# Kernel optimization log

Hardware: AMD Instinct MI355X
Metric: run time of the kernel (lower is better)

## Reference

```python
import jax, jax.numpy as jnp
import numpy as np
from jax import lax

T, B, A = 128, 32, 18  # rollout steps, num envs, action dim
HID = 128
FEAT = 512


def _conv(x, w, b, stride):
    y = lax.conv_general_dilated(x, w, (stride, stride), 'VALID',
                                 dimension_numbers=('NCHW', 'OIHW', 'NCHW'))
    return y + b[None, :, None, None]


def setup_inputs() -> dict:
    key = jax.random.key(0)
    ks = jax.random.split(key, 16)

    def w(k, shape, fan_in):
        return jax.random.normal(k, shape, dtype=jnp.float32) / np.sqrt(fan_in)

    x = jax.random.uniform(ks[0], (T * B, 4, 84, 84), dtype=jnp.float32) * 255.0
    done = jax.random.randint(ks[1], (T * B,), 0, 2, dtype=jnp.int32)
    h0 = jax.random.normal(ks[2], (1, B, HID), dtype=jnp.float32) * 0.1
    c0 = jax.random.normal(ks[3], (1, B, HID), dtype=jnp.float32) * 0.1
    return {
        'x': x, 'done': done, 'h0': h0, 'c0': c0,
        'w1': w(ks[4], (32, 4, 8, 8), 4 * 64), 'b1': jnp.zeros((32,), jnp.float32),
        'w2': w(ks[5], (64, 32, 4, 4), 32 * 16), 'b2': jnp.zeros((64,), jnp.float32),
        'w3': w(ks[6], (64, 64, 3, 3), 64 * 9), 'b3': jnp.zeros((64,), jnp.float32),
        'wf': w(ks[7], (FEAT, 3136), 3136), 'bf': jnp.zeros((FEAT,), jnp.float32),
        'w_ih': w(ks[8], (4 * HID, FEAT), FEAT), 'w_hh': w(ks[9], (4 * HID, HID), HID),
        'b_ih': jnp.zeros((4 * HID,), jnp.float32), 'b_hh': jnp.zeros((4 * HID,), jnp.float32),
        'wa': w(ks[10], (A, HID), HID) * 0.01, 'ba': jnp.zeros((A,), jnp.float32),
        'wc': w(ks[11], (1, HID), HID), 'bc': jnp.zeros((1,), jnp.float32),
    }


def reference(x, done, h0, c0, w1, b1, w2, b2, w3, b3, wf, bf,
              w_ih, w_hh, b_ih, b_hh, wa, ba, wc, bc):
    # Nature-CNN trunk on x/255
    h = jax.nn.relu(_conv(x / 255.0, w1, b1, 4))   # (TB,32,20,20)
    h = jax.nn.relu(_conv(h, w2, b2, 2))           # (TB,64,9,9)
    h = jax.nn.relu(_conv(h, w3, b3, 1))           # (TB,64,7,7)
    h = h.reshape(h.shape[0], -1)                   # (TB,3136)
    feat = jax.nn.relu(h @ wf.T + bf)               # (TB,512)

    xs = feat.reshape(T, B, FEAT)
    ds = done.reshape(T, B).astype(feat.dtype)

    def step(carry, inp):
        hh, cc = carry
        xt, dt = inp
        m = (1.0 - dt)[:, None]      # done-mask reset of recurrent state
        hh = hh * m
        cc = cc * m
        gates = xt @ w_ih.T + b_ih + hh @ w_hh.T + b_hh
        i, f, g, o = jnp.split(gates, 4, axis=-1)  # torch LSTM gate order
        cc = jax.nn.sigmoid(f) * cc + jax.nn.sigmoid(i) * jnp.tanh(g)
        hh = jax.nn.sigmoid(o) * jnp.tanh(cc)
        return (hh, cc), hh

    (_, _), hs = lax.scan(step, (h0[0], c0[0]), (xs, ds))
    hidden = hs.reshape(T * B, HID)

    logits = hidden @ wa.T + ba                     # actor head
    value = hidden @ wc.T + bc                      # critic head
    return jnp.concatenate([logits, value], axis=-1)  # (TB, A+1)
```

## Files before the change

### kernel.cpp

```cpp
#include <hip/hip_runtime.h>

typedef _Float16 f16;
typedef _Float16 f16x2 __attribute__((ext_vector_type(2)));
typedef _Float16 f16x4 __attribute__((ext_vector_type(4)));
typedef _Float16 f16x8 __attribute__((ext_vector_type(8)));
typedef float f32x4 __attribute__((ext_vector_type(4)));

__device__ __forceinline__ float sigf(float x){ return 1.f/(1.f + __expf(-x)); }
__device__ __forceinline__ float tanhfast(float x){ return 2.f/(1.f + __expf(-2.f*x)) - 1.f; }
__device__ __forceinline__ float fdot2f(f16x2 a, f16x2 b, float c){
#if __has_builtin(__builtin_amdgcn_fdot2)
  return __builtin_amdgcn_fdot2(a, b, c, false);
#else
  return c + (float)a.x*(float)b.x + (float)a.y*(float)b.y;
#endif
}

__global__ void prep_w1(const float* __restrict__ w, f16* __restrict__ dst){
  int idx = blockIdx.x*256 + threadIdx.x;
  if (idx >= 8192) return;
  int och = idx >> 8, rem = idx & 255;
  int c = rem >> 6, ky = (rem >> 3) & 7, kx = rem & 7;
  int k = c*64 + ky*8 + kx;
  dst[(k>>3)*256 + och*8 + (k&7)] = (f16)(w[idx] * (1.f/255.f));
}
__global__ void prep_w2(const float* __restrict__ w, f16* __restrict__ dst){
  int idx = blockIdx.x*256 + threadIdx.x;
  if (idx >= 32768) return;
  int och = idx >> 9;
  int c = (idx >> 4) & 31, ky = (idx >> 2) & 3, kx = idx & 3;
  int k = (ky*4 + kx)*32 + c;
  dst[(k>>3)*512 + och*8 + (k&7)] = (f16)w[idx];
}
__global__ void prep_w3(const float* __restrict__ w, f16* __restrict__ dst){
  int idx = blockIdx.x*256 + threadIdx.x;
  if (idx >= 36864) return;
  int och = idx / 576, r = idx % 576;
  int c = r / 9, r2 = r % 9;
  int ky = r2 / 3, kx = r2 % 3;
  int k = (ky*3 + kx)*64 + c;
  dst[(k>>3)*512 + och*8 + (k&7)] = (f16)w[idx];
}
__global__ void prep_wf(const float* __restrict__ w, f16* __restrict__ dst){
  int idx = blockIdx.x*256 + threadIdx.x;
  if (idx >= 392*512*8) return;
  int j = idx & 7, n = (idx >> 3) & 511, k8 = idx >> 12;
  int kf = k8*8 + j;
  int c = kf & 63, p = kf >> 6;
  dst[idx] = (f16)w[(size_t)n*3136 + c*49 + p];
}
__global__ void prep_wih(const float* __restrict__ w, f16* __restrict__ dst){
  int idx = blockIdx.x*256 + threadIdx.x;
  if (idx >= 262144) return;
  int j = idx & 7, n = (idx >> 3) & 511, k8 = idx >> 12;
  dst[idx] = (f16)w[n*512 + k8*8 + j];
}
__global__ void prep_wheads(const float* __restrict__ wa, const float* __restrict__ wc,
                            f16* __restrict__ dst){
  int idx = blockIdx.x*256 + threadIdx.x;
  if (idx >= 4096) return;
  int n = idx >> 7, k = idx & 127;
  float v = 0.f;
  if (n < 18) v = wa[n*128 + k];
  else if (n == 18) v = wc[k];
  dst[(k>>3)*256 + n*8 + (k&7)] = (f16)v;
}
__global__ void prep_bsum(const float* __restrict__ a, const float* __restrict__ b,
                          float* __restrict__ s){
  int i = blockIdx.x*256 + threadIdx.x;
  if (i < 512) s[i] = a[i] + b[i];
}
__global__ void prep_whh(const float* __restrict__ w, f16* __restrict__ dst){
  int idx = blockIdx.x*256 + threadIdx.x;
  if (idx >= 65536) return;
  int nn = idx >> 7, k = idx & 127;
  dst[(k >> 1)*1024 + nn*2 + (k & 1)] = (f16)w[idx];
}

__global__ __launch_bounds__(256, 3) void conv123_k(const float* __restrict__ x,
    const f16* __restrict__ Bp1, const float* __restrict__ b1,
    const f16* __restrict__ Bp2, const float* __restrict__ b2,
    const f16* __restrict__ Bp3, const float* __restrict__ b3,
    f16* __restrict__ y3){
  __shared__ alignas(16) f16 xt[4*24*84];
  __shared__ alignas(16) f16 y1t[400*32];
  int n = blockIdx.x;
  int tid = threadIdx.x;
  int lane = tid & 63, w = tid >> 6;
  int q = lane >> 4, m = lane & 15;

  int wg = w & 1, wm = w >> 1;
  int och1 = wg*16 + m;
  f16x8 bfr1[8];
  #pragma unroll
  for (int s = 0; s < 8; ++s)
    bfr1[s] = *(const f16x8*)(Bp1 + ((4*s + q)*32 + och1)*8);
  float bias1 = b1[och1];

  #pragma unroll
  for (int h = 0; h < 4; ++h){
    for (int i = tid; i < 2016; i += 256){
      int c = i / 504, r = i % 504;
      int iy = r / 21, x4 = r % 21;
      const float4* xp = (const float4*)(x + (((size_t)n*4 + c)*84 + h*20 + iy)*84) + x4;
      float4 v = *xp;
      f16x4 hv = { (f16)v.x, (f16)v.y, (f16)v.z, (f16)v.w };
      *(f16x4*)(&xt[(c*24 + iy)*84 + x4*4]) = hv;
    }
    __syncthreads();
    int oy4[4], ox4[4];
    #pragma unroll
    for (int i = 0; i < 4; ++i){
      int pl = i*16 + m; if (pl > 49) pl = 49;
      int p = wm*50 + pl;
      oy4[i] = (p/20)*4; ox4[i] = (p%20)*4;
    }
    f32x4 acc1[4] = {};
    #pragma unroll
    for (int s = 0; s < 8; ++s){
      int k8 = 4*s + q;
      int c = k8 >> 3, ky = k8 & 7;
      #pragma unroll
      for (int i = 0; i < 4; ++i){
        const f16* ap = &xt[(c*24 + oy4[i] + ky)*84 + ox4[i]];
        f16x4 lo = *(const f16x4*)ap;
        f16x4 hi = *(const f16x4*)(ap + 4);
        f16x8 a = __builtin_shufflevector(lo, hi, 0,1,2,3,4,5,6,7);
        acc1[i] = __builtin_amdgcn_mfma_f32_16x16x32_f16(a, bfr1[s], acc1[i], 0, 0, 0);
      }
    }
    #pragma unroll
    for (int i = 0; i < 4; ++i)
      #pragma unroll
      for (int r = 0; r < 4; ++r){
        int pl = i*16 + q*4 + r;
        if (pl < 50){
          int P = h*100 + wm*50 + pl;
          float v = acc1[i][r] + bias1; v = v > 0.f ? v : 0.f;
          int idx = (P*32 + och1) ^ (((P>>1)&7)<<3);
          y1t[idx] = (f16)v;
        }
      }
    __syncthreads();
  }

  int och2 = w*16 + m;
  f16x8 bfr2[16];
  #pragma unroll
  for (int s = 0; s < 16; ++s)
    bfr2[s] = *(const f16x8*)(Bp2 + ((size_t)(4*s + q)*64 + och2)*8);
  int basev[6];
  #pragma unroll
  for (int i = 0; i < 6; ++i){
    int px = i*16 + m; if (px > 80) px = 80;
    basev[i] = (px/9*2)*20 + (px%9)*2;
  }
  f32x4 acc2[6] = {};
  #pragma unroll
  for (int s = 0; s < 16; ++s){
    int k8 = 4*s + q;
    int c0 = (k8 & 3)*8;
    int kk = k8 >> 2;
    int poff = (kk >> 2)*20 + (kk & 3);
    #pragma unroll
    for (int i = 0; i < 6; ++i){
      int p = basev[i] + poff;
      int idx = (p*32 + c0) ^ (((p>>1)&7)<<3);
      f16x8 a = *(const f16x8*)(&y1t[idx]);
      acc2[i] = __builtin_amdgcn_mfma_f32_16x16x32_f16(a, bfr2[s], acc2[i], 0, 0, 0);
    }
  }
  float bias2 = b2[och2];
  #pragma unroll
  for (int i = 0; i < 6; ++i)
    #pragma unroll
    for (int r = 0; r < 4; ++r){
      int px = i*16 + q*4 + r;
      if (px < 81){
        float v = acc2[i][r] + bias2; v = v > 0.f ? v : 0.f;
        int idx = (px*64 + och2) ^ ((px&7)<<3);
        xt[idx] = (f16)v;
      }
    }
  __syncthreads();

  int basev3[4];
  #pragma unroll
  for (int i = 0; i < 4; ++i){
    int px = i*16 + m; if (px > 48) px = 48;
    basev3[i] = (px/7)*9 + (px%7);
  }
  f32x4 acc3[4] = {};
  for (int s = 0; s < 18; ++s){
    int k8 = 4*s + q;
    int c0 = (k8 & 7)*8;
    int kxy = k8 >> 3;
    int ky = kxy/3, kx = kxy%3;
    f16x8 b = *(const f16x8*)(Bp3 + ((size_t)k8*64 + och2)*8);
    int poff = ky*9 + kx;
    #pragma unroll
    for (int i = 0; i < 4; ++i){
      int p = basev3[i] + poff;
      int idx = (p*64 + c0) ^ ((p&7)<<3);
      f16x8 a = *(const f16x8*)(&xt[idx]);
      acc3[i] = __builtin_amdgcn_mfma_f32_16x16x32_f16(a, b, acc3[i], 0, 0, 0);
    }
  }
  float bias3 = b3[och2];
  #pragma unroll
  for (int i = 0; i < 4; ++i)
    #pragma unroll
    for (int r = 0; r < 4; ++r){
      int px = i*16 + q*4 + r;
      if (px < 49){
        float v = acc3[i][r] + bias3; v = v > 0.f ? v : 0.f;
        y3[((size_t)n*49 + px)*64 + och2] = (f16)v;
      }
    }
}

template<bool RELU, bool OUTH>
__global__ __launch_bounds__(256) void gemm_k(const f16* __restrict__ A,
    const f16* __restrict__ Bp, const float* __restrict__ bias, void* __restrict__ out,
    int M, int N, int K){
  __shared__ alignas(16) f16 at[64*264];
  int m0 = blockIdx.x*64, n0 = blockIdx.y*64;
  int lane = threadIdx.x & 63, w = threadIdx.x >> 6;
  int q = lane >> 4, cl = lane & 15;
  int mh = w >> 1, nh = w & 1;
  f32x4 acc[2][2] = {};
  for (int kb = 0; kb < K; kb += 256){
    int kblen = K - kb; if (kblen > 256) kblen = 256;
    int c8n = kblen >> 3;
    __syncthreads();
    int tot = 64*c8n;
    for (int i = threadIdx.x; i < tot; i += 256){
      int row, c8;
      if (c8n == 32){ row = i >> 5; c8 = i & 31; } else { row = i >> 3; c8 = i & 7; }
      *(f16x8*)(&at[row*264 + c8*8]) = *(const f16x8*)(&A[(size_t)(m0+row)*K + kb + c8*8]);
    }
    __syncthreads();
    int nks = kblen >> 5;
    for (int s = 0; s < nks; ++s){
      f16x8 a[2], b[2];
      #pragma unroll
      for (int mi = 0; mi < 2; ++mi)
        a[mi] = *(const f16x8*)(&at[((mh*2+mi)*16 + cl)*264 + 32*s + 8*q]);
      #pragma unroll
      for (int ni = 0; ni < 2; ++ni){
        int nn = n0 + (nh*2+ni)*16 + cl;
        b[ni] = *(const f16x8*)(&Bp[((size_t)((kb>>3) + 4*s + q)*N + nn)*8]);
      }
      #pragma unroll
      for (int mi = 0; mi < 2; ++mi)
        #pragma unroll
        for (int ni = 0; ni < 2; ++ni)
          acc[mi][ni] = __builtin_amdgcn_mfma_f32_16x16x32_f16(a[mi], b[ni], acc[mi][ni], 0,0,0);
    }
  }
  #pragma unroll
  for (int ni = 0; ni < 2; ++ni){
    int nn = n0 + (nh*2+ni)*16 + cl;
    float bv = bias[nn];
    #pragma unroll
    for (int mi = 0; mi < 2; ++mi)
      #pragma unroll
      for (int r = 0; r < 4; ++r){
        int mg = m0 + (mh*2+mi)*16 + q*4 + r;
        float v = acc[mi][ni][r] + bv;
        if (RELU) v = v > 0.f ? v : 0.f;
        if (OUTH) ((f16*)out)[(size_t)mg*N + nn] = (f16)v;
        else      ((float*)out)[(size_t)mg*N + nn] = v;
      }
  }
}

__global__ __launch_bounds__(128) void lstm_seg(const float* __restrict__ gx,
    const f16* __restrict__ whhT2, const int* __restrict__ done,
    const float* __restrict__ h0, const float* __restrict__ c0,
    f16* __restrict__ hs){
  int e = blockIdx.y, t0 = blockIdx.x;
  if (t0 > 0 && done[t0*32 + e] == 0) return;
  int j = threadIdx.x;
  __shared__ f16 hl[2][128];
  float h, c;
  if (t0 == 0){
    float mm = 1.f - (float)done[e];
    h = h0[e*128 + j]*mm;
    c = c0[e*128 + j]*mm;
  } else { h = 0.f; c = 0.f; }
  int buf = 0;
  hl[0][j] = (f16)h;
  __syncthreads();
  const f16x2* wp = (const f16x2*)whhT2;
  for (int t = t0; t < 128; ++t){
    if (t > t0 && done[t*32 + e] != 0) break;
    const float* gxr = gx + ((size_t)t*32 + e)*512;
    float gi = gxr[j], gf = gxr[128 + j], gg = gxr[256 + j], go = gxr[384 + j];
    const f16x2* hp = (const f16x2*)hl[buf];
    float ai = 0.f, af = 0.f, ag = 0.f, ao = 0.f;
    #pragma unroll 8
    for (int k2 = 0; k2 < 64; ++k2){
      f16x2 hv = hp[k2];
      const f16x2* wr = wp + k2*512;
      ai = fdot2f(wr[j], hv, ai);
      af = fdot2f(wr[128 + j], hv, af);
      ag = fdot2f(wr[256 + j], hv, ag);
      ao = fdot2f(wr[384 + j], hv, ao);
    }
    gi += ai; gf += af; gg += ag; go += ao;
    c = sigf(gf)*c + sigf(gi)*tanhfast(gg);
    h = sigf(go)*tanhfast(c);
    hs[((size_t)t*32 + e)*128 + j] = (f16)h;
    buf ^= 1;
    hl[buf][j] = (f16)h;
    __syncthreads();
  }
}

__global__ __launch_bounds__(256) void heads_k(const f16* __restrict__ hs,
    const f16* __restrict__ Bp, const float* __restrict__ ba, const float* __restrict__ bc,
    float* __restrict__ out){
  __shared__ alignas(16) f16 at[64*128];
  int m0 = blockIdx.x*64;
  for (int i = threadIdx.x; i < 1024; i += 256)
    ((uint4*)at)[i] = ((const uint4*)(hs + (size_t)m0*128))[i];
  int lane = threadIdx.x & 63, w = threadIdx.x >> 6;
  int q = lane >> 4, cl = lane & 15;
  __syncthreads();
  f32x4 acc[2] = {};
  #pragma unroll
  for (int s = 0; s < 4; ++s){
    f16x8 a = *(const f16x8*)(&at[(w*16 + cl)*128 + 32*s + 8*q]);
    #pragma unroll
    for (int nt = 0; nt < 2; ++nt){
      f16x8 b = *(const f16x8*)(&Bp[((4*s + q)*32 + nt*16 + cl)*8]);
      acc[nt] = __builtin_amdgcn_mfma_f32_16x16x32_f16(a, b, acc[nt], 0,0,0);
    }
  }
  #pragma unroll
  for (int nt = 0; nt < 2; ++nt){
    int n = nt*16 + cl;
    if (n < 19){
      float bv = (n < 18) ? ba[n] : bc[0];
      #pragma unroll
      for (int r = 0; r < 4; ++r){
        int m = m0 + w*16 + q*4 + r;
        out[(size_t)m*19 + n] = acc[nt][r] + bv;
      }
    }
  }
}

extern "C" void kernel_launch(void* const* d_in, const int* in_sizes, int n_in,
                              void* d_out, int out_size, void* d_ws, size_t ws_size,
                              hipStream_t stream){
  const float* x   = (const float*)d_in[0];
  const int*   dn  = (const int*)d_in[1];
  const float* h0  = (const float*)d_in[2];
  const float* c0  = (const float*)d_in[3];
  const float* w1  = (const float*)d_in[4];
  const float* b1  = (const float*)d_in[5];
  const float* w2  = (const float*)d_in[6];
  const float* b2  = (const float*)d_in[7];
  const float* w3  = (const float*)d_in[8];
  const float* b3  = (const float*)d_in[9];
  const float* wf  = (const float*)d_in[10];
  const float* bf  = (const float*)d_in[11];
  const float* wih = (const float*)d_in[12];
  const float* whh = (const float*)d_in[13];
  const float* bih = (const float*)d_in[14];
  const float* bhh = (const float*)d_in[15];
  const float* wa  = (const float*)d_in[16];
  const float* ba  = (const float*)d_in[17];
  const float* wc  = (const float*)d_in[18];
  const float* bc  = (const float*)d_in[19];
  float* out = (float*)d_out;

  char* ws = (char*)d_ws;
  size_t off = 0;
  auto alloc = [&](size_t bytes)->char*{
    char* p = ws + off;
    off += (bytes + 255) & ~(size_t)255;
    return p;
  };
  f16*  y3   = (f16*)alloc(4096UL*3136*2);
  f16*  feat = (f16*)alloc(4096UL*512*2);
  float* gx  = (float*)alloc(4096UL*512*4);
  f16*  hs   = (f16*)alloc(4096UL*128*2);
  f16*  Bp1  = (f16*)alloc(32UL*32*8*2);
  f16*  Bp2  = (f16*)alloc(64UL*64*8*2);
  f16*  Bp3  = (f16*)alloc(72UL*64*8*2);
  f16*  Bpf  = (f16*)alloc(392UL*512*8*2);
  f16*  Bpih = (f16*)alloc(64UL*512*8*2);
  f16*  Bph  = (f16*)alloc(16UL*32*8*2);
  float* bsum = (float*)alloc(512UL*4);
  f16*  whhT2 = (f16*)alloc(64UL*512*2*2);

  prep_w1<<<32, 256, 0, stream>>>(w1, Bp1);
  prep_w2<<<128, 256, 0, stream>>>(w2, Bp2);
  prep_w3<<<144, 256, 0, stream>>>(w3, Bp3);
  prep_wf<<<6272, 256, 0, stream>>>(wf, Bpf);
  prep_wih<<<1024, 256, 0, stream>>>(wih, Bpih);
  prep_wheads<<<16, 256, 0, stream>>>(wa, wc, Bph);
  prep_bsum<<<2, 256, 0, stream>>>(bih, bhh, bsum);
  prep_whh<<<256, 256, 0, stream>>>(whh, whhT2);

  conv123_k<<<4096, 256, 0, stream>>>(x, Bp1, b1, Bp2, b2, Bp3, b3, y3);
  gemm_k<true,  true ><<<dim3(64, 8), 256, 0, stream>>>(y3,   Bpf,  bf,   (void*)feat, 4096, 512, 3136);
  gemm_k<false, false><<<dim3(64, 8), 256, 0, stream>>>(feat, Bpih, bsum, (void*)gx,   4096, 512, 512);
  lstm_seg<<<dim3(128, 32), 128, 0, stream>>>(gx, whhT2, dn, h0, c0, hs);
  heads_k<<<64, 256, 0, stream>>>(hs, Bph, ba, bc, out);
}
```

Baseline: 897.6 us.

## Prefetch conv1 input bands into registers and vectorize conv epilogue stores

The fused conv kernel now loads the next 20-row input band into registers while the current band is computed, so global-load latency overlaps MFMA work instead of stalling each band. MFMA operands are swapped so each lane holds four consecutive output channels, which lets the bias+ReLU epilogues write packed f16x4 to LDS and global memory instead of scalar f16 stores. The cost is 8 float4 registers per thread held across the loop, which may pressure occupancy at launch bounds of 3 blocks.

```diff
diff --git a/kernel.cpp b/kernel.cpp
--- a/kernel.cpp
+++ b/kernel.cpp
@@ -88,32 +88,52 @@
   int tid = threadIdx.x;
   int lane = tid & 63, w = tid >> 6;
   int q = lane >> 4, m = lane & 15;
-
   int wg = w & 1, wm = w >> 1;
+  const float* xn = x + (size_t)n*4*84*84;
+
+  float4 fl[8];
+  #pragma unroll
+  for (int u = 0; u < 8; ++u){
+    int i = tid + u*256; if (i > 2015) i = 2015;
+    int c = i / 504, r = i % 504;
+    int iy = r / 21, x4 = r % 21;
+    fl[u] = *((const float4*)(xn + (c*84 + iy)*84) + x4);
+  }
   int och1 = wg*16 + m;
   f16x8 bfr1[8];
   #pragma unroll
   for (int s = 0; s < 8; ++s)
     bfr1[s] = *(const f16x8*)(Bp1 + ((4*s + q)*32 + och1)*8);
-  float bias1 = b1[och1];
+  f32x4 bias1v = *(const f32x4*)(b1 + wg*16 + q*4);
 
   #pragma unroll
   for (int h = 0; h < 4; ++h){
-    for (int i = tid; i < 2016; i += 256){
+    __syncthreads();
+    #pragma unroll
+    for (int u = 0; u < 8; ++u){
+      int i = tid + u*256; if (i > 2015) i = 2015;
       int c = i / 504, r = i % 504;
       int iy = r / 21, x4 = r % 21;
-      const float4* xp = (const float4*)(x + (((size_t)n*4 + c)*84 + h*20 + iy)*84) + x4;
-      float4 v = *xp;
+      float4 v = fl[u];
       f16x4 hv = { (f16)v.x, (f16)v.y, (f16)v.z, (f16)v.w };
       *(f16x4*)(&xt[(c*24 + iy)*84 + x4*4]) = hv;
     }
+    if (h < 3){
+      #pragma unroll
+      for (int u = 0; u < 8; ++u){
+        int i = tid + u*256; if (i > 2015) i = 2015;
+        int c = i / 504, r = i % 504;
+        int iy = r / 21, x4 = r % 21;
+        fl[u] = *((const float4*)(xn + (c*84 + (h+1)*20 + iy)*84) + x4);
+      }
+    }
     __syncthreads();
     int oy4[4], ox4[4];
     #pragma unroll
-    for (int i = 0; i < 4; ++i){
-      int pl = i*16 + m; if (pl > 49) pl = 49;
+    for (int i2 = 0; i2 < 4; ++i2){
+      int pl = i2*16 + m; if (pl > 49) pl = 49;
       int p = wm*50 + pl;
-      oy4[i] = (p/20)*4; ox4[i] = (p%20)*4;
+      oy4[i2] = (p/20)*4; ox4[i2] = (p%20)*4;
     }
     f32x4 acc1[4] = {};
     #pragma unroll
@@ -121,28 +141,31 @@
       int k8 = 4*s + q;
       int c = k8 >> 3, ky = k8 & 7;
       #pragma unroll
-      for (int i = 0; i < 4; ++i){
-        const f16* ap = &xt[(c*24 + oy4[i] + ky)*84 + ox4[i]];
+      for (int i2 = 0; i2 < 4; ++i2){
+        const f16* ap = &xt[(c*24 + oy4[i2] + ky)*84 + ox4[i2]];
         f16x4 lo = *(const f16x4*)ap;
         f16x4 hi = *(const f16x4*)(ap + 4);
         f16x8 a = __builtin_shufflevector(lo, hi, 0,1,2,3,4,5,6,7);
-        acc1[i] = __builtin_amdgcn_mfma_f32_16x16x32_f16(a, bfr1[s], acc1[i], 0, 0, 0);
-      }
-    }
-    #pragma unroll
-    for (int i = 0; i < 4; ++i)
-      #pragma unroll
-      for (int r = 0; r < 4; ++r){
-        int pl = i*16 + q*4 + r;
-        if (pl < 50){
-          int P = h*100 + wm*50 + pl;
-          float v = acc1[i][r] + bias1; v = v > 0.f ? v : 0.f;
-          int idx = (P*32 + och1) ^ (((P>>1)&7)<<3);
-          y1t[idx] = (f16)v;
+        acc1[i2] = __builtin_amdgcn_mfma_f32_16x16x32_f16(bfr1[s], a, acc1[i2], 0, 0, 0);
+      }
+    }
+    #pragma unroll
+    for (int i2 = 0; i2 < 4; ++i2){
+      int pl = i2*16 + m;
+      if (pl < 50){
+        int P = h*100 + wm*50 + pl;
+        f16x4 hv;
+        #pragma unroll
+        for (int r = 0; r < 4; ++r){
+          float v = acc1[i2][r] + bias1v[r]; v = v > 0.f ? v : 0.f;
+          hv[r] = (f16)v;
         }
-      }
-    __syncthreads();
-  }
+        int idx = (P*32 + wg*16 + q*4) ^ (((P>>1)&7)<<3);
+        *(f16x4*)(&y1t[idx]) = hv;
+      }
+    }
+  }
+  __syncthreads();
 
   int och2 = w*16 + m;
   f16x8 bfr2[16];
@@ -167,21 +190,24 @@
       int p = basev[i] + poff;
       int idx = (p*32 + c0) ^ (((p>>1)&7)<<3);
       f16x8 a = *(const f16x8*)(&y1t[idx]);
-      acc2[i] = __builtin_amdgcn_mfma_f32_16x16x32_f16(a, bfr2[s], acc2[i], 0, 0, 0);
-    }
-  }
-  float bias2 = b2[och2];
-  #pragma unroll
-  for (int i = 0; i < 6; ++i)
-    #pragma unroll
-    for (int r = 0; r < 4; ++r){
-      int px = i*16 + q*4 + r;
-      if (px < 81){
-        float v = acc2[i][r] + bias2; v = v > 0.f ? v : 0.f;
-        int idx = (px*64 + och2) ^ ((px&7)<<3);
-        xt[idx] = (f16)v;
-      }
-    }
+      acc2[i] = __builtin_amdgcn_mfma_f32_16x16x32_f16(bfr2[s], a, acc2[i], 0, 0, 0);
+    }
+  }
+  f32x4 bias2v = *(const f32x4*)(b2 + w*16 + q*4);
+  #pragma unroll
+  for (int i = 0; i < 6; ++i){
+    int px = i*16 + m;
+    if (px < 81){
+      f16x4 hv;
+      #pragma unroll
+      for (int r = 0; r < 4; ++r){
+        float v = acc2[i][r] + bias2v[r]; v = v > 0.f ? v : 0.f;
+        hv[r] = (f16)v;
+      }
+      int idx = (px*64 + w*16 + q*4) ^ ((px&7)<<3);
+      *(f16x4*)(&xt[idx]) = hv;
+    }
+  }
   __syncthreads();
 
   int basev3[4];
@@ -203,20 +229,23 @@
       int p = basev3[i] + poff;
       int idx = (p*64 + c0) ^ ((p&7)<<3);
       f16x8 a = *(const f16x8*)(&xt[idx]);
-      acc3[i] = __builtin_amdgcn_mfma_f32_16x16x32_f16(a, b, acc3[i], 0, 0, 0);
-    }
-  }
-  float bias3 = b3[och2];
-  #pragma unroll
-  for (int i = 0; i < 4; ++i)
-    #pragma unroll
-    for (int r = 0; r < 4; ++r){
-      int px = i*16 + q*4 + r;
-      if (px < 49){
-        float v = acc3[i][r] + bias3; v = v > 0.f ? v : 0.f;
-        y3[((size_t)n*49 + px)*64 + och2] = (f16)v;
-      }
-    }
+      acc3[i] = __builtin_amdgcn_mfma_f32_16x16x32_f16(b, a, acc3[i], 0, 0, 0);
+    }
+  }
+  f32x4 bias3v = *(const f32x4*)(b3 + w*16 + q*4);
+  #pragma unroll
+  for (int i = 0; i < 4; ++i){
+    int px = i*16 + m;
+    if (px < 49){
+      f16x4 hv;
+      #pragma unroll
+      for (int r = 0; r < 4; ++r){
+        float v = acc3[i][r] + bias3v[r]; v = v > 0.f ? v : 0.f;
+        hv[r] = (f16)v;
+      }
+      *(f16x4*)(&y3[((size_t)n*49 + px)*64 + w*16 + q*4]) = hv;
+    }
+  }
 }
 
 template<bool RELU, bool OUTH>
```

Measured after the change: 844.0 us. 6.0% less time.
